# Kernel tuning notes

Measured on AMD Instinct MI355X. Metric: run time of the kernel, lower is better.

The kernel has to match this reference:

```python
import jax, jax.numpy as jnp
import numpy as np
import math

HIDDEN = 1024
HEADS = 16
HEAD_DIM = HIDDEN // HEADS


def setup_inputs() -> dict:
    key = jax.random.key(0)
    ks = jax.random.split(key, 9)
    B, T, C = 4, 2048, HIDDEN
    s = 0.02
    x = jax.random.normal(ks[0], (B, T, C), dtype=jnp.float32)
    # torch nn.Linear weights are [out_features, in_features]
    Wq = jax.random.normal(ks[1], (C, C), dtype=jnp.float32) * s
    Wk = jax.random.normal(ks[2], (C, C), dtype=jnp.float32) * s
    Wv = jax.random.normal(ks[3], (C, C), dtype=jnp.float32) * s
    Wo = jax.random.normal(ks[4], (C, C), dtype=jnp.float32) * s
    bq = jax.random.normal(ks[5], (C,), dtype=jnp.float32) * s
    bk = jax.random.normal(ks[6], (C,), dtype=jnp.float32) * s
    bv = jax.random.normal(ks[7], (C,), dtype=jnp.float32) * s
    bo = jax.random.normal(ks[8], (C,), dtype=jnp.float32) * s
    return {"x": x, "Wq": Wq, "bq": bq, "Wk": Wk, "bk": bk,
            "Wv": Wv, "bv": bv, "Wo": Wo, "bo": bo}


def reference(x, Wq, bq, Wk, bk, Wv, bv, Wo, bo):
    B, T, C = x.shape
    H, D = HEADS, HEAD_DIM
    # projections: torch Linear => x @ W.T + b
    q = (x @ Wq.T + bq).reshape(B, T, H, D).transpose(0, 2, 1, 3)  # [B,H,T,D]
    k = (x @ Wk.T + bk).reshape(B, T, H, D).transpose(0, 2, 1, 3)
    v = (x @ Wv.T + bv).reshape(B, T, H, D).transpose(0, 2, 1, 3)
    scale = 1.0 / math.sqrt(D)
    scores = jnp.einsum('bhqd,bhkd->bhqk', q, k) * scale  # [B,H,T,T]
    attn = jax.nn.softmax(scores, axis=-1)
    y = jnp.einsum('bhqk,bhkd->bhqd', attn, v)  # [B,H,T,D]
    y = y.transpose(0, 2, 1, 3).reshape(B, T, C)
    return y @ Wo.T + bo
```

## Files before the change

kernel.cpp:

```cpp
#include <hip/hip_runtime.h>
#include <stdint.h>


using u16 = unsigned short;
using u32 = unsigned int;
typedef __attribute__((ext_vector_type(8))) __bf16 bf16x8;
typedef __attribute__((ext_vector_type(4))) float  floatx4;

#define QSCALE 0.18033688011112043f

__device__ __forceinline__ u16 f2b(float f) {
    union { float f; u32 i; } x; x.f = f;
    return (u16)((x.i + 0x7fffu + ((x.i >> 16) & 1u)) >> 16);
}
__device__ __forceinline__ u32 fbits(float f) { union { float f; u32 i; } x; x.f = f; return x.i; }
__device__ __forceinline__ u32 pkbf(float a, float b) {
    u32 ia = fbits(a) + 0x8000u, ib = fbits(b) + 0x8000u;
    return __builtin_amdgcn_perm(ib, ia, 0x07060302u);
}
__device__ __forceinline__ bf16x8 ld16B(const u16* p) {
    bf16x8 v; __builtin_memcpy(&v, p, 16); return v;
}
__device__ __forceinline__ void async16(const u16* g, u16* l) {
    __builtin_amdgcn_global_load_lds((const __attribute__((address_space(1))) unsigned int*)g,
                                     (__attribute__((address_space(3))) unsigned int*)l,
                                     16, 0, 0);
}

__global__ __launch_bounds__(256) void convert_kernel(
    const float* __restrict__ x,
    const float* __restrict__ Wq, const float* __restrict__ Wk,
    const float* __restrict__ Wv, const float* __restrict__ Wo,
    u16* __restrict__ xb, u16* __restrict__ wqb, u16* __restrict__ wkb,
    u16* __restrict__ wvb, u16* __restrict__ wob)
{
    size_t e = ((size_t)blockIdx.x * 256 + threadIdx.x) * 4;
    const float* src; u16* dst; size_t off;
    const size_t XN = (size_t)8 << 20;
    if (e < XN) { src = x; dst = xb; off = e; }
    else {
        size_t k = e - XN;
        int w = (int)(k >> 20);
        off = k & ((1u << 20) - 1);
        src = (w == 0) ? Wq : (w == 1) ? Wk : (w == 2) ? Wv : Wo;
        dst = (w == 0) ? wqb : (w == 1) ? wkb : (w == 2) ? wvb : wob;
    }
    float4 f = *(const float4*)(src + off);
    u32 dws[2] = { pkbf(f.x, f.y), pkbf(f.z, f.w) };
    __builtin_memcpy(dst + off, dws, 8);
}

__device__ __forceinline__ void gemm_loop(const u16* __restrict__ A, const u16* __restrict__ W,
                                          int m0, int n0, floatx4 (&acc)[4][4],
                                          u16* __restrict__ sA, u16* __restrict__ sB)
{
    constexpr int K = 1024;
    const int tid  = threadIdx.x;
    const int wave = tid >> 6, lane = tid & 63;
    const int wr = wave >> 1, wc = wave & 1;
    const int quad = lane >> 4, l15 = lane & 15;

    #pragma unroll
    for (int i = 0; i < 4; ++i)
        #pragma unroll
        for (int j = 0; j < 4; ++j)
            acc[i][j] = (floatx4){0.f, 0.f, 0.f, 0.f};

    const int rstage = lane >> 3;
    const int gstage = lane & 7;

    #pragma unroll 1
    for (int kb = 0; kb < 16; ++kb) {
        __syncthreads();
        const int k0 = kb * 64;
        #pragma unroll
        for (int j = 0; j < 4; ++j) {
            int r  = wave * 32 + j * 8 + rstage;
            int kg = gstage ^ (r & 7);
            async16(A + (size_t)(m0 + r) * K + k0 + kg * 8, &sA[(wave * 32 + j * 8) * 64]);
            async16(W + (size_t)(n0 + r) * K + k0 + kg * 8, &sB[(wave * 32 + j * 8) * 64]);
        }
        __syncthreads();

        #pragma unroll
        for (int kk = 0; kk < 2; ++kk) {
            bf16x8 af[4], bf[4];
            const int kg = kk * 4 + quad;
            #pragma unroll
            for (int t = 0; t < 4; ++t) {
                int ra = wr * 64 + t * 16 + l15;
                af[t] = ld16B(&sA[ra * 64 + ((kg ^ (ra & 7)) * 8)]);
                int rb = wc * 64 + t * 16 + l15;
                bf[t] = ld16B(&sB[rb * 64 + ((kg ^ (rb & 7)) * 8)]);
            }
            #pragma unroll
            for (int mt = 0; mt < 4; ++mt)
                #pragma unroll
                for (int nt = 0; nt < 4; ++nt)
                    acc[mt][nt] = __builtin_amdgcn_mfma_f32_16x16x32_bf16(af[mt], bf[nt], acc[mt][nt], 0, 0, 0);
        }
    }
}

__global__ __launch_bounds__(256, 3) void qkv_kernel(
    const u16* __restrict__ x, const u16* __restrict__ Wcat,
    const float* __restrict__ bq, const float* __restrict__ bk, const float* __restrict__ bv,
    u16* __restrict__ q, u16* __restrict__ k, u16* __restrict__ vt)
{
    __shared__ __align__(16) u16 sA[128 * 64];
    __shared__ __align__(16) u16 sB[128 * 64];
    const int id = blockIdx.x;
    const int xcd = id & 7, slot = id >> 3;
    const int m0 = (xcd * 8 + (slot & 7)) * 128;
    const int n0 = (slot >> 3) * 128;
    floatx4 acc[4][4];
    gemm_loop(x, Wcat, m0, n0, acc, sA, sB);

    const int tid = threadIdx.x;
    const int wave = tid >> 6, lane = tid & 63;
    const int wr = wave >> 1, wc = wave & 1;
    const int quad = lane >> 4, l15 = lane & 15;

    const int z = n0 >> 10;
    const float* bb = (z == 0) ? bq : (z == 1) ? bk : bv;
    const float scale = (z == 0) ? QSCALE : 1.0f;
    u16* o = (z == 0) ? q : k;

    #pragma unroll
    for (int nt = 0; nt < 4; ++nt) {
        int col  = n0 + wc * 64 + nt * 16 + l15;
        int c    = col & 1023;
        float bv_ = bb[c];
        #pragma unroll
        for (int mt = 0; mt < 4; ++mt) {
            int row0 = m0 + wr * 64 + mt * 16 + quad * 4;
            if (z == 2) {
                float v0 = acc[mt][nt][0] + bv_, v1 = acc[mt][nt][1] + bv_;
                float v2 = acc[mt][nt][2] + bv_, v3 = acc[mt][nt][3] + bv_;
                u32 dws[2] = { pkbf(v0, v1), pkbf(v2, v3) };
                int b = row0 >> 11, t0 = row0 & 2047;
                size_t idx = ((size_t)((b * 16 + (c >> 6)) * 64 + (c & 63)) * 2048) + t0;
                __builtin_memcpy(vt + idx, dws, 8);
            } else {
                #pragma unroll
                for (int r = 0; r < 4; ++r) {
                    float v = (acc[mt][nt][r] + bv_) * scale;
                    o[(size_t)(row0 + r) * 1024 + c] = f2b(v);
                }
            }
        }
    }
}

__global__ __launch_bounds__(256, 3) void proj_kernel(
    const u16* __restrict__ y, const u16* __restrict__ Wo, const float* __restrict__ bo,
    float* __restrict__ out)
{
    __shared__ __align__(16) u16 sA[128 * 64];
    __shared__ __align__(16) u16 sB[128 * 64];
    const int id = blockIdx.x;
    const int xcd = id & 7, slot = id >> 3;
    const int m0 = (xcd * 8 + (slot & 7)) * 128;
    const int n0 = (slot >> 3) * 128;
    floatx4 acc[4][4];
    gemm_loop(y, Wo, m0, n0, acc, sA, sB);

    const int tid = threadIdx.x;
    const int wave = tid >> 6, lane = tid & 63;
    const int wr = wave >> 1, wc = wave & 1;
    const int quad = lane >> 4, l15 = lane & 15;

    #pragma unroll
    for (int nt = 0; nt < 4; ++nt) {
        int col = n0 + wc * 64 + nt * 16 + l15;
        float bv_ = bo[col];
        #pragma unroll
        for (int mt = 0; mt < 4; ++mt) {
            int row0 = m0 + wr * 64 + mt * 16 + quad * 4;
            #pragma unroll
            for (int r = 0; r < 4; ++r)
                out[(size_t)(row0 + r) * 1024 + col] = acc[mt][nt][r] + bv_;
        }
    }
}

__global__ __launch_bounds__(256, 2) void attn_kernel(
    const u16* __restrict__ Q, const u16* __restrict__ K,
    const u16* __restrict__ Vt, u16* __restrict__ Y)
{
    const int bh = blockIdx.x, qt = blockIdx.y;
    const int tid = threadIdx.x;
    const int wave = tid >> 6, lane = tid & 63;
    const int quad = lane >> 4, l15 = lane & 15, l7 = l15 & 7;
    const int b = bh >> 4, h = bh & 15;

    __shared__ __align__(16) u16 sK[2][64 * 64];
    __shared__ __align__(16) u16 sV[2][64 * 64];
    __shared__ __align__(16) u16 sP[4][64 * 72];

    const __bf16 one = (__bf16)1.0f;
    const bf16x8 ones = { one, one, one, one, one, one, one, one };

    bf16x8 qf[4][2];
    #pragma unroll
    for (int nt = 0; nt < 4; ++nt) {
        const u16* qp = Q + (size_t)(b * 2048 + qt * 256 + wave * 64 + nt * 16 + l15) * 1024 + h * 64 + quad * 8;
        qf[nt][0] = ld16B(qp);
        qf[nt][1] = ld16B(qp + 32);
    }

    const int r8 = lane >> 3;
    const int g7 = (lane & 7) ^ r8;
    const u16* ksrc = K  + (size_t)(b * 2048 + wave * 16 + r8) * 1024 + h * 64 + g7 * 8;
    const u16* vsrc = Vt + ((size_t)(bh * 64 + wave * 16 + r8)) * 2048 + g7 * 8;

    floatx4 accO[4][4];
    #pragma unroll
    for (int mt = 0; mt < 4; ++mt)
        #pragma unroll
        for (int nt = 0; nt < 4; ++nt) accO[mt][nt] = (floatx4){0.f, 0.f, 0.f, 0.f};
    floatx4 accR[4];
    #pragma unroll
    for (int nt = 0; nt < 4; ++nt) accR[nt] = (floatx4){0.f, 0.f, 0.f, 0.f};

    {
        u16* dK = &sK[0][wave * 16 * 64];
        u16* dV = &sV[0][wave * 16 * 64];
        async16(ksrc,            dK);
        async16(ksrc + 8 * 1024, dK + 8 * 64);
        async16(vsrc,            dV);
        async16(vsrc + 8 * 2048, dV + 8 * 64);
    }
    __syncthreads();

    u16* sp = sP[wave];
    const int spRow = l15 * 72;

    #pragma unroll 1
    for (int kt = 0; kt < 32; ++kt) {
        const int cur = kt & 1;
        if (kt < 31) {
            u16* dK = &sK[cur ^ 1][wave * 16 * 64];
            u16* dV = &sV[cur ^ 1][wave * 16 * 64];
            const u16* ks = ksrc + (size_t)(kt + 1) * 64 * 1024;
            const u16* vs = vsrc + (size_t)(kt + 1) * 64;
            async16(ks,            dK);
            async16(ks + 8 * 1024, dK + 8 * 64);
            async16(vs,            dV);
            async16(vs + 8 * 2048, dV + 8 * 64);
        }
        const u16* bK = sK[cur];
        const u16* bV = sV[cur];

        bf16x8 kf[4][2], vf[4][2];
        #pragma unroll
        for (int mt = 0; mt < 4; ++mt)
            #pragma unroll
            for (int kk = 0; kk < 2; ++kk) {
                kf[mt][kk] = ld16B(&bK[(mt * 16 + l15) * 64 + (((kk * 4 + quad) ^ l7) * 8)]);
                vf[mt][kk] = ld16B(&bV[(mt * 16 + l15) * 64 + (((kk * 4 + quad) ^ l7) * 8)]);
            }

        #pragma unroll
        for (int nt = 0; nt < 4; ++nt) {
            floatx4 st[4];
            #pragma unroll
            for (int mt = 0; mt < 4; ++mt) st[mt] = (floatx4){0.f, 0.f, 0.f, 0.f};
            #pragma unroll
            for (int kk = 0; kk < 2; ++kk)
                #pragma unroll
                for (int mt = 0; mt < 4; ++mt)
                    st[mt] = __builtin_amdgcn_mfma_f32_16x16x32_bf16(kf[mt][kk], qf[nt][kk], st[mt], 0, 0, 0);

            u16* spn = sp + nt * 16 * 72 + spRow;
            #pragma unroll
            for (int mt = 0; mt < 4; ++mt) {
                float p0 = __builtin_amdgcn_exp2f(st[mt][0]);
                float p1 = __builtin_amdgcn_exp2f(st[mt][1]);
                float p2 = __builtin_amdgcn_exp2f(st[mt][2]);
                float p3 = __builtin_amdgcn_exp2f(st[mt][3]);
                u32 dws[2] = { pkbf(p0, p1), pkbf(p2, p3) };
                __builtin_memcpy(spn + mt * 16 + quad * 4, dws, 8);
            }
            bf16x8 pf0 = ld16B(spn + quad * 8);
            bf16x8 pf1 = ld16B(spn + 32 + quad * 8);
            accR[nt] = __builtin_amdgcn_mfma_f32_16x16x32_bf16(ones, pf0, accR[nt], 0, 0, 0);
            accR[nt] = __builtin_amdgcn_mfma_f32_16x16x32_bf16(ones, pf1, accR[nt], 0, 0, 0);
            #pragma unroll
            for (int mt = 0; mt < 4; ++mt) {
                accO[mt][nt] = __builtin_amdgcn_mfma_f32_16x16x32_bf16(vf[mt][0], pf0, accO[mt][nt], 0, 0, 0);
                accO[mt][nt] = __builtin_amdgcn_mfma_f32_16x16x32_bf16(vf[mt][1], pf1, accO[mt][nt], 0, 0, 0);
            }
        }
        __syncthreads();
    }

    float inv[4];
    #pragma unroll
    for (int nt = 0; nt < 4; ++nt) inv[nt] = 1.f / accR[nt][0];
    #pragma unroll
    for (int nt = 0; nt < 4; ++nt)
        #pragma unroll
        for (int mt = 0; mt < 4; ++mt) {
            u32 dws[2] = { pkbf(accO[mt][nt][0] * inv[nt], accO[mt][nt][1] * inv[nt]),
                           pkbf(accO[mt][nt][2] * inv[nt], accO[mt][nt][3] * inv[nt]) };
            __builtin_memcpy(&sp[(nt * 16 + l15) * 72 + mt * 16 + quad * 4], dws, 8);
        }
    const int rl = lane >> 3, cl = lane & 7;
    #pragma unroll
    for (int pass = 0; pass < 8; ++pass) {
        int qq = pass * 8 + rl;
        int t = qt * 256 + wave * 64 + qq;
        bf16x8 vrow = ld16B(&sp[qq * 72 + cl * 8]);
        __builtin_memcpy(Y + ((size_t)(b * 2048 + t)) * 1024 + h * 64 + cl * 8, &vrow, 16);
    }
}

extern "C" void kernel_launch(void* const* d_in, const int* in_sizes, int n_in,
                              void* d_out, int out_size, void* d_ws, size_t ws_size,
                              hipStream_t stream)
{
    const float* x  = (const float*)d_in[0];
    const float* Wq = (const float*)d_in[1];
    const float* bq = (const float*)d_in[2];
    const float* Wk = (const float*)d_in[3];
    const float* bk = (const float*)d_in[4];
    const float* Wv = (const float*)d_in[5];
    const float* bv = (const float*)d_in[6];
    const float* Wo = (const float*)d_in[7];
    const float* bo = (const float*)d_in[8];
    float* out = (float*)d_out;

    const size_t NTOK = (size_t)8192 * 1024;
    const size_t WN   = (size_t)1024 * 1024;
    u16* xb  = (u16*)d_ws;
    u16* wqb = xb + NTOK;
    u16* wkb = wqb + WN;
    u16* wvb = wkb + WN;
    u16* wob = wvb + WN;
    u16* q   = wob + WN;
    u16* k   = q + NTOK;
    u16* vt  = k + NTOK;
    u16* y   = vt + NTOK;

    convert_kernel<<<dim3(12288), 256, 0, stream>>>(x, Wq, Wk, Wv, Wo, xb, wqb, wkb, wvb, wob);
    qkv_kernel<<<dim3(1536), 256, 0, stream>>>(xb, wqb, bq, bk, bv, q, k, vt);
    attn_kernel<<<dim3(64, 8), 256, 0, stream>>>(q, k, vt, y);
    proj_kernel<<<dim3(512), 256, 0, stream>>>(y, wob, bo, out);
}
```

Before: 248.3 us.

## Rework attention inner loop with 32x32 MFMA and register-resident P via permlane swap

The attention kernel moves from 16x16x32 to 32x32x16 bf16 MFMA tiles. The softmax probabilities are now packed with v_cvt_pk_bf16_f32 and rearranged in registers with permlane32_swap, so they no longer round-trip through shared memory. The row sum is accumulated with scalar adds instead of extra MFMAs against a ones vector, and s_setprio is raised around the MFMA blocks. This removes LDS traffic and the redundant sum MFMAs, at the cost of larger accumulator register pressure and a fragile lane-layout mapping.

```diff
diff --git a/kernel.cpp b/kernel.cpp
--- a/kernel.cpp
+++ b/kernel.cpp
@@ -4,8 +4,10 @@
 
 using u16 = unsigned short;
 using u32 = unsigned int;
-typedef __attribute__((ext_vector_type(8))) __bf16 bf16x8;
-typedef __attribute__((ext_vector_type(4))) float  floatx4;
+typedef __attribute__((ext_vector_type(8)))  __bf16 bf16x8;
+typedef __attribute__((ext_vector_type(4)))  float  floatx4;
+typedef __attribute__((ext_vector_type(16))) float  f32x16;
+typedef __attribute__((ext_vector_type(2)))  unsigned int u32x2;
 
 #define QSCALE 0.18033688011112043f
 
@@ -17,6 +19,9 @@
 __device__ __forceinline__ u32 pkbf(float a, float b) {
     u32 ia = fbits(a) + 0x8000u, ib = fbits(b) + 0x8000u;
     return __builtin_amdgcn_perm(ib, ia, 0x07060302u);
+}
+__device__ __forceinline__ u32 cvtpk(float a, float b) {
+    u32 r; asm("v_cvt_pk_bf16_f32 %0, %1, %2" : "=v"(r) : "v"(a), "v"(b)); return r;
 }
 __device__ __forceinline__ bf16x8 ld16B(const u16* p) {
     bf16x8 v; __builtin_memcpy(&v, p, 16); return v;
@@ -191,22 +196,19 @@
     const int bh = blockIdx.x, qt = blockIdx.y;
     const int tid = threadIdx.x;
     const int wave = tid >> 6, lane = tid & 63;
-    const int quad = lane >> 4, l15 = lane & 15, l7 = l15 & 7;
+    const int hf = lane >> 5, l31 = lane & 31, l7 = l31 & 7;
     const int b = bh >> 4, h = bh & 15;
 
-    __shared__ __align__(16) u16 sK[2][64 * 64];
-    __shared__ __align__(16) u16 sV[2][64 * 64];
-    __shared__ __align__(16) u16 sP[4][64 * 72];
-
-    const __bf16 one = (__bf16)1.0f;
-    const bf16x8 ones = { one, one, one, one, one, one, one, one };
-
-    bf16x8 qf[4][2];
-    #pragma unroll
-    for (int nt = 0; nt < 4; ++nt) {
-        const u16* qp = Q + (size_t)(b * 2048 + qt * 256 + wave * 64 + nt * 16 + l15) * 1024 + h * 64 + quad * 8;
-        qf[nt][0] = ld16B(qp);
-        qf[nt][1] = ld16B(qp + 32);
+    __shared__ __align__(16) u16 smem[16384];
+
+    bf16x8 qf[2][4];
+    {
+        const size_t q0 = (size_t)(b * 2048 + qt * 256 + wave * 64) * 1024 + h * 64 + hf * 8;
+        #pragma unroll
+        for (int nq = 0; nq < 2; ++nq)
+            #pragma unroll
+            for (int dc = 0; dc < 4; ++dc)
+                qf[nq][dc] = ld16B(Q + q0 + (size_t)(nq * 32 + l31) * 1024 + dc * 16);
     }
 
     const int r8 = lane >> 3;
@@ -214,104 +216,133 @@
     const u16* ksrc = K  + (size_t)(b * 2048 + wave * 16 + r8) * 1024 + h * 64 + g7 * 8;
     const u16* vsrc = Vt + ((size_t)(bh * 64 + wave * 16 + r8)) * 2048 + g7 * 8;
 
-    floatx4 accO[4][4];
-    #pragma unroll
-    for (int mt = 0; mt < 4; ++mt)
-        #pragma unroll
-        for (int nt = 0; nt < 4; ++nt) accO[mt][nt] = (floatx4){0.f, 0.f, 0.f, 0.f};
-    floatx4 accR[4];
-    #pragma unroll
-    for (int nt = 0; nt < 4; ++nt) accR[nt] = (floatx4){0.f, 0.f, 0.f, 0.f};
+    f32x16 accO[2][2];
+    #pragma unroll
+    for (int dt = 0; dt < 2; ++dt)
+        #pragma unroll
+        for (int nq = 0; nq < 2; ++nq)
+            #pragma unroll
+            for (int i = 0; i < 16; ++i) accO[dt][nq][i] = 0.f;
+    float accS[2] = {0.f, 0.f};
 
     {
-        u16* dK = &sK[0][wave * 16 * 64];
-        u16* dV = &sV[0][wave * 16 * 64];
+        u16* dK = smem + wave * 1024;
+        u16* dV = smem + 8192 + wave * 1024;
         async16(ksrc,            dK);
-        async16(ksrc + 8 * 1024, dK + 8 * 64);
+        async16(ksrc + 8 * 1024, dK + 512);
         async16(vsrc,            dV);
-        async16(vsrc + 8 * 2048, dV + 8 * 64);
+        async16(vsrc + 8 * 2048, dV + 512);
     }
     __syncthreads();
-
-    u16* sp = sP[wave];
-    const int spRow = l15 * 72;
 
     #pragma unroll 1
     for (int kt = 0; kt < 32; ++kt) {
         const int cur = kt & 1;
         if (kt < 31) {
-            u16* dK = &sK[cur ^ 1][wave * 16 * 64];
-            u16* dV = &sV[cur ^ 1][wave * 16 * 64];
+            u16* dK = smem + (cur ^ 1) * 4096 + wave * 1024;
+            u16* dV = smem + 8192 + (cur ^ 1) * 4096 + wave * 1024;
             const u16* ks = ksrc + (size_t)(kt + 1) * 64 * 1024;
             const u16* vs = vsrc + (size_t)(kt + 1) * 64;
             async16(ks,            dK);
-            async16(ks + 8 * 1024, dK + 8 * 64);
+            async16(ks + 8 * 1024, dK + 512);
             async16(vs,            dV);
-            async16(vs + 8 * 2048, dV + 8 * 64);
-        }
-        const u16* bK = sK[cur];
-        const u16* bV = sV[cur];
-
-        bf16x8 kf[4][2], vf[4][2];
-        #pragma unroll
-        for (int mt = 0; mt < 4; ++mt)
-            #pragma unroll
-            for (int kk = 0; kk < 2; ++kk) {
-                kf[mt][kk] = ld16B(&bK[(mt * 16 + l15) * 64 + (((kk * 4 + quad) ^ l7) * 8)]);
-                vf[mt][kk] = ld16B(&bV[(mt * 16 + l15) * 64 + (((kk * 4 + quad) ^ l7) * 8)]);
+            async16(vs + 8 * 2048, dV + 512);
+        }
+        const u16* bK = smem + cur * 4096;
+        const u16* bV = smem + 8192 + cur * 4096;
+
+        bf16x8 kfm[2][4];
+        #pragma unroll
+        for (int m = 0; m < 2; ++m) {
+            const int row = m * 32 + l31;
+            #pragma unroll
+            for (int dc = 0; dc < 4; ++dc)
+                kfm[m][dc] = ld16B(&bK[row * 64 + (((dc * 2 + hf) ^ l7) * 8)]);
+        }
+
+        f32x16 st[2][2];
+        #pragma unroll
+        for (int m = 0; m < 2; ++m)
+            #pragma unroll
+            for (int nq = 0; nq < 2; ++nq)
+                #pragma unroll
+                for (int i = 0; i < 16; ++i) st[m][nq][i] = 0.f;
+        __builtin_amdgcn_s_setprio(1);
+        #pragma unroll
+        for (int dc = 0; dc < 4; ++dc)
+            #pragma unroll
+            for (int m = 0; m < 2; ++m)
+                #pragma unroll
+                for (int nq = 0; nq < 2; ++nq)
+                    st[m][nq] = __builtin_amdgcn_mfma_f32_32x32x16_bf16(kfm[m][dc], qf[nq][dc], st[m][nq], 0, 0, 0);
+        __builtin_amdgcn_s_setprio(0);
+
+        bf16x8 vfm[2][4];
+        #pragma unroll
+        for (int dt = 0; dt < 2; ++dt) {
+            const int row = dt * 32 + l31;
+            #pragma unroll
+            for (int c = 0; c < 4; ++c)
+                vfm[dt][c] = ld16B(&bV[row * 64 + (((c * 2 + hf) ^ l7) * 8)]);
+        }
+
+        #pragma unroll
+        for (int c = 0; c < 4; ++c) {
+            const int m = c >> 1, r0 = (c & 1) * 8;
+            #pragma unroll
+            for (int nq = 0; nq < 2; ++nq) {
+                float e0 = __builtin_amdgcn_exp2f(st[m][nq][r0 + 0]);
+                float e1 = __builtin_amdgcn_exp2f(st[m][nq][r0 + 1]);
+                float e2 = __builtin_amdgcn_exp2f(st[m][nq][r0 + 2]);
+                float e3 = __builtin_amdgcn_exp2f(st[m][nq][r0 + 3]);
+                float e4 = __builtin_amdgcn_exp2f(st[m][nq][r0 + 4]);
+                float e5 = __builtin_amdgcn_exp2f(st[m][nq][r0 + 5]);
+                float e6 = __builtin_amdgcn_exp2f(st[m][nq][r0 + 6]);
+                float e7 = __builtin_amdgcn_exp2f(st[m][nq][r0 + 7]);
+                accS[nq] += ((e0 + e1) + (e2 + e3)) + ((e4 + e5) + (e6 + e7));
+                u32 Ua = cvtpk(e0, e1), Ub = cvtpk(e2, e3);
+                u32 Va = cvtpk(e4, e5), Vb = cvtpk(e6, e7);
+                u32x2 s0 = __builtin_amdgcn_permlane32_swap(Ua, Va, false, false);
+                u32x2 s1 = __builtin_amdgcn_permlane32_swap(Ub, Vb, false, false);
+                u32 dws[4] = { s0.x, s1.x, s0.y, s1.y };
+                bf16x8 pB; __builtin_memcpy(&pB, dws, 16);
+                __builtin_amdgcn_s_setprio(1);
+                accO[0][nq] = __builtin_amdgcn_mfma_f32_32x32x16_bf16(vfm[0][c], pB, accO[0][nq], 0, 0, 0);
+                accO[1][nq] = __builtin_amdgcn_mfma_f32_32x32x16_bf16(vfm[1][c], pB, accO[1][nq], 0, 0, 0);
+                __builtin_amdgcn_s_setprio(0);
             }
-
-        #pragma unroll
-        for (int nt = 0; nt < 4; ++nt) {
-            floatx4 st[4];
-            #pragma unroll
-            for (int mt = 0; mt < 4; ++mt) st[mt] = (floatx4){0.f, 0.f, 0.f, 0.f};
-            #pragma unroll
-            for (int kk = 0; kk < 2; ++kk)
-                #pragma unroll
-                for (int mt = 0; mt < 4; ++mt)
-                    st[mt] = __builtin_amdgcn_mfma_f32_16x16x32_bf16(kf[mt][kk], qf[nt][kk], st[mt], 0, 0, 0);
-
-            u16* spn = sp + nt * 16 * 72 + spRow;
-            #pragma unroll
-            for (int mt = 0; mt < 4; ++mt) {
-                float p0 = __builtin_amdgcn_exp2f(st[mt][0]);
-                float p1 = __builtin_amdgcn_exp2f(st[mt][1]);
-                float p2 = __builtin_amdgcn_exp2f(st[mt][2]);
-                float p3 = __builtin_amdgcn_exp2f(st[mt][3]);
-                u32 dws[2] = { pkbf(p0, p1), pkbf(p2, p3) };
-                __builtin_memcpy(spn + mt * 16 + quad * 4, dws, 8);
+        }
+        __syncthreads();
+    }
+
+    #pragma unroll
+    for (int nq = 0; nq < 2; ++nq) accS[nq] += __shfl_xor(accS[nq], 32);
+    const float inv0 = 1.f / accS[0], inv1 = 1.f / accS[1];
+
+    u16* ep = smem + wave * 4096;
+    #pragma unroll
+    for (int nq = 0; nq < 2; ++nq) {
+        const float inv = nq ? inv1 : inv0;
+        const int row = nq * 32 + l31;
+        #pragma unroll
+        for (int dt = 0; dt < 2; ++dt)
+            #pragma unroll
+            for (int rq = 0; rq < 4; ++rq) {
+                float v0 = accO[dt][nq][rq * 4 + 0] * inv;
+                float v1 = accO[dt][nq][rq * 4 + 1] * inv;
+                float v2 = accO[dt][nq][rq * 4 + 2] * inv;
+                float v3 = accO[dt][nq][rq * 4 + 3] * inv;
+                u32 dws[2] = { cvtpk(v0, v1), cvtpk(v2, v3) };
+                const int g = dt * 4 + rq;
+                __builtin_memcpy((char*)ep + row * 128 + ((g ^ l7) * 16) + hf * 8, dws, 8);
             }
-            bf16x8 pf0 = ld16B(spn + quad * 8);
-            bf16x8 pf1 = ld16B(spn + 32 + quad * 8);
-            accR[nt] = __builtin_amdgcn_mfma_f32_16x16x32_bf16(ones, pf0, accR[nt], 0, 0, 0);
-            accR[nt] = __builtin_amdgcn_mfma_f32_16x16x32_bf16(ones, pf1, accR[nt], 0, 0, 0);
-            #pragma unroll
-            for (int mt = 0; mt < 4; ++mt) {
-                accO[mt][nt] = __builtin_amdgcn_mfma_f32_16x16x32_bf16(vf[mt][0], pf0, accO[mt][nt], 0, 0, 0);
-                accO[mt][nt] = __builtin_amdgcn_mfma_f32_16x16x32_bf16(vf[mt][1], pf1, accO[mt][nt], 0, 0, 0);
-            }
-        }
-        __syncthreads();
-    }
-
-    float inv[4];
-    #pragma unroll
-    for (int nt = 0; nt < 4; ++nt) inv[nt] = 1.f / accR[nt][0];
-    #pragma unroll
-    for (int nt = 0; nt < 4; ++nt)
-        #pragma unroll
-        for (int mt = 0; mt < 4; ++mt) {
-            u32 dws[2] = { pkbf(accO[mt][nt][0] * inv[nt], accO[mt][nt][1] * inv[nt]),
-                           pkbf(accO[mt][nt][2] * inv[nt], accO[mt][nt][3] * inv[nt]) };
-            __builtin_memcpy(&sp[(nt * 16 + l15) * 72 + mt * 16 + quad * 4], dws, 8);
-        }
+    }
     const int rl = lane >> 3, cl = lane & 7;
     #pragma unroll
     for (int pass = 0; pass < 8; ++pass) {
-        int qq = pass * 8 + rl;
-        int t = qt * 256 + wave * 64 + qq;
-        bf16x8 vrow = ld16B(&sp[qq * 72 + cl * 8]);
+        const int row = pass * 8 + rl;
+        bf16x8 vrow = ld16B((const u16*)((const char*)ep + row * 128 + ((cl ^ rl) * 16)));
+        const int t = qt * 256 + wave * 64 + row;
         __builtin_memcpy(Y + ((size_t)(b * 2048 + t)) * 1024 + h * 64 + cl * 8, &vrow, 16);
     }
 }
```

Measured after the change: 263.7 us. +6.2%, slower.
